# Performance work log

Hardware: AMD Instinct MI355X
Metric: run time of the kernel (lower is better)

## Reference

```python
import jax, jax.numpy as jnp
import numpy as np
from jax import lax

B, T, C = 512, 128, 66
H, L, W = 512, 2, 10


def gru_cell(x, h, W_ih, W_hh, b_ih, b_hh):
    # PyTorch GRU gate order: r, z, n
    gi = x @ W_ih.T + b_ih            # [B, 3H]
    gh = h @ W_hh.T + b_hh            # [B, 3H]
    i_r, i_z, i_n = jnp.split(gi, 3, axis=-1)
    h_r, h_z, h_n = jnp.split(gh, 3, axis=-1)
    r = jax.nn.sigmoid(i_r + h_r)
    z = jax.nn.sigmoid(i_z + h_z)
    n = jnp.tanh(i_n + r * h_n)
    return (1.0 - z) * n + z * h


def setup_inputs() -> dict:
    key = jax.random.key(0)
    ks = jax.random.split(key, 16)
    s = 0.02
    inp = {
        "x": jax.random.normal(ks[0], (B, T, C), jnp.float32),
        # GRU layer 0 (input C -> hidden H)
        "W_ih0": jax.random.normal(ks[1], (3 * H, C), jnp.float32) * s,
        "W_hh0": jax.random.normal(ks[2], (3 * H, H), jnp.float32) * s,
        "b_ih0": jnp.zeros((3 * H,), jnp.float32),
        "b_hh0": jnp.zeros((3 * H,), jnp.float32),
        # GRU layer 1 (hidden H -> hidden H)
        "W_ih1": jax.random.normal(ks[3], (3 * H, H), jnp.float32) * s,
        "W_hh1": jax.random.normal(ks[4], (3 * H, H), jnp.float32) * s,
        "b_ih1": jnp.zeros((3 * H,), jnp.float32),
        "b_hh1": jnp.zeros((3 * H,), jnp.float32),
        # temporal_fc: Linear(window_size, 1) -> weight [1, W], bias [1]
        "temporal_w": jax.random.normal(ks[5], (1, W), jnp.float32) * s,
        "temporal_b": jnp.zeros((1,), jnp.float32),
        # spatial_fc: Linear(H, C)
        "spatial_w": jax.random.normal(ks[6], (C, H), jnp.float32) * s,
        "spatial_b": jnp.zeros((C,), jnp.float32),
    }
    return inp


def _forward(x, W_ih0, W_hh0, b_ih0, b_hh0, W_ih1, W_hh1, b_ih1, b_hh1,
             temporal_w, temporal_b, spatial_w, spatial_b):
    p0 = (W_ih0, W_hh0, b_ih0, b_hh0)
    p1 = (W_ih1, W_hh1, b_ih1, b_hh1)

    # ---- encoder: 2-layer GRU over the full sequence ----
    xs = jnp.transpose(x, (1, 0, 2))  # [T, B, C]
    h0 = jnp.zeros((x.shape[0], H), x.dtype)

    def make_step(p):
        def step(h, xt):
            hn = gru_cell(xt, h, *p)
            return hn, hn
        return step

    hT0, ys0 = lax.scan(make_step(p0), h0, xs)          # ys0 [T,B,H]
    hT1, ys1 = lax.scan(make_step(p1), h0, ys0)         # ys1 [T,B,H]

    encoder_window = jnp.transpose(ys1[-W:], (1, 0, 2))  # [B, W, H]
    last_input_frame = x[:, -1, :]                       # [B, C]

    def dec_step(carry, _):
        (h_0, h_1), win, dec_in = carry
        h_0n = gru_cell(dec_in, h_0, *p0)
        h_1n = gru_cell(h_0n, h_1, *p1)                  # decoder_out [B,H]
        win = jnp.concatenate([win[:, 1:, :], h_1n[:, None, :]], axis=1)
        # temporal_fc over window axis: [B,W,H] -> [B,H]
        t = jnp.einsum('bwh,w->bh', win, temporal_w[0]) + temporal_b[0]
        frame = t @ spatial_w.T + spatial_b + dec_in     # recursive residual
        return ((h_0n, h_1n), win, frame), frame

    init = ((hT0, hT1), encoder_window, last_input_frame)
    _, frames = lax.scan(dec_step, init, None, length=T)  # [T,B,C]
    return jnp.transpose(frames, (1, 0, 2))               # [B,T,C]


def reference(x, W_ih0, W_hh0, b_ih0, b_hh0, W_ih1, W_hh1, b_ih1, b_hh1,
              temporal_w, temporal_b, spatial_w, spatial_b):
    return _forward(x, W_ih0, W_hh0, b_ih0, b_hh0, W_ih1, W_hh1, b_ih1, b_hh1,
                    temporal_w, temporal_b, spatial_w, spatial_b)
```

## Files before the change

### kernel.cpp

```cpp
#include <hip/hip_runtime.h>
#include <hip/hip_bf16.h>

typedef __attribute__((ext_vector_type(8))) short bf16x8;
typedef __attribute__((ext_vector_type(4))) float f32x4;

#define NB 512
#define NT 128
#define NC 66
#define NH 512
#define NW 10
#define CP 96
#define BM 32
#define BJ 64
#define BK 32
#define BKP 40
#define NWG 256
#define NTHR 256
#define G3 1536

struct Params {
  const float *x, *Wih0, *Whh0, *bih0, *bhh0, *Wih1, *Whh1, *bih1, *bhh1, *tw, *tb, *sw, *sb;
  float *out;
  unsigned *barL, *barG;
  __hip_bfloat16 *Wih0h, *Wih0l;
  __hip_bfloat16 *Wch, *Wcl;
  float *cb;
  float *h0, *h1, *tvec;
  __hip_bfloat16 *winb;
};

__device__ __forceinline__ float sigmoidf_(float x) { return 1.f / (1.f + __expf(-x)); }
__device__ __forceinline__ float tanhf_(float x) {
  float e = __expf(2.f * x);
  return (e - 1.f) / (e + 1.f);
}
__device__ __forceinline__ void split2(float v, __hip_bfloat16& h, __hip_bfloat16& l) {
  h = __float2bfloat16(v);
  l = __float2bfloat16(v - __bfloat162float(h));
}
__device__ __forceinline__ unsigned short bfbits(__hip_bfloat16 h) { return *(unsigned short*)&h; }
__device__ __forceinline__ void splitpack4(float4 v, ushort4& ph, ushort4& pl) {
  __hip_bfloat16 h, l;
  split2(v.x, h, l); ph.x = bfbits(h); pl.x = bfbits(l);
  split2(v.y, h, l); ph.y = bfbits(h); pl.y = bfbits(l);
  split2(v.z, h, l); ph.z = bfbits(h); pl.z = bfbits(l);
  split2(v.w, h, l); ph.w = bfbits(h); pl.w = bfbits(l);
}

__device__ __forceinline__ float4 cload4(const float* p) {
  unsigned long long a = __hip_atomic_load((const unsigned long long*)p,       __ATOMIC_RELAXED, __HIP_MEMORY_SCOPE_AGENT);
  unsigned long long b = __hip_atomic_load(((const unsigned long long*)p) + 1, __ATOMIC_RELAXED, __HIP_MEMORY_SCOPE_AGENT);
  float4 r;
  ((unsigned long long*)&r)[0] = a;
  ((unsigned long long*)&r)[1] = b;
  return r;
}

__device__ __forceinline__ void gbar(unsigned* barL, unsigned* barG, unsigned& phase,
                                     int tid, int grp) {
  __syncthreads();
  ++phase;
  if (tid == 0) {
    unsigned old = __hip_atomic_fetch_add(&barL[grp * 32], 1u, __ATOMIC_RELEASE,
                                          __HIP_MEMORY_SCOPE_AGENT);
    if (old == phase * 32 - 1)
      __hip_atomic_fetch_add(barG, 1u, __ATOMIC_RELAXED, __HIP_MEMORY_SCOPE_AGENT);
    while (__hip_atomic_load(barG, __ATOMIC_RELAXED, __HIP_MEMORY_SCOPE_AGENT) < phase)
      __builtin_amdgcn_s_sleep(2);
  }
  __syncthreads();
  asm volatile("" ::: "memory");
}

#define AM_X 0
#define AM_H 2

__device__ __forceinline__ float4 loadA(int amode, const float* __restrict__ A, int tstep,
                                        int b0, int am, int k) {
  if (amode == AM_X) {
    const float* xr = A + ((size_t)(b0 + am) * NT + tstep) * NC;
    float4 v;
    v.x = (k + 0 < NC) ? xr[k + 0] : 0.f;
    v.y = (k + 1 < NC) ? xr[k + 1] : 0.f;
    v.z = (k + 2 < NC) ? xr[k + 2] : 0.f;
    v.w = (k + 3 < NC) ? xr[k + 3] : 0.f;
    return v;
  }
  return cload4(A + (size_t)(b0 + am) * NH + k);
}

__device__ __forceinline__ void zacc(f32x4 acc[2][4]) {
#pragma unroll
  for (int i = 0; i < 2; ++i)
#pragma unroll
    for (int g = 0; g < 4; ++g) {
      acc[i][g][0] = 0.f; acc[i][g][1] = 0.f; acc[i][g][2] = 0.f; acc[i][g][3] = 0.f;
    }
}

template <int G2, bool PSW>
__device__ __forceinline__ void gemm_tile(
    f32x4 acc[2][4],
    const __hip_bfloat16* __restrict__ Wh, const __hip_bfloat16* __restrict__ Wl,
    const float* __restrict__ Wf, int Kb,
    int amode, const float* __restrict__ A, int tstep,
    int b0, int j0,
    __hip_bfloat16* AsH, __hip_bfloat16* AsL,
    __hip_bfloat16* BsH, __hip_bfloat16* BsL,
    int tid)
{
  const int wv = tid >> 6, lane = tid & 63, quad = lane >> 4, l15 = lane & 15;
  const int ms = wv & 1, jh = wv >> 1;
  const int am = tid >> 3;
  const int ak = (tid & 7) << 2;
  const int nk = Kb >> 5;

  uint4 bh_[3], bl_[3];
  float4 w0_[3], w1_[3];

  auto fetchB = [&](int st) {
    const int kb = st << 5;
#pragma unroll
    for (int r = 0; r < 3; ++r) {
      const int l = tid + r * NTHR;
      const int nl = l >> 2, k8 = (l & 3) << 3;
      const int g = nl >> 6, jl = nl & 63;
      if (PSW) {
        const size_t o = (size_t)(g * NH + j0 + jl) * Kb + kb + k8;
        bh_[r] = *(const uint4*)(Wh + o);
        bl_[r] = *(const uint4*)(Wl + o);
      } else {
        const float* wp = Wf + (size_t)(g * NH + j0 + jl) * Kb + kb + k8;
        w0_[r] = *(const float4*)wp;
        w1_[r] = *(const float4*)(wp + 4);
      }
    }
  };

  float4 av = loadA(amode, A, tstep, b0, am, ak);
  fetchB(0);

  for (int st = 0; st < nk; ++st) {
    const int cur = st & 1;
    __hip_bfloat16* ah_d = AsH + cur * (BM * BKP);
    __hip_bfloat16* al_d = AsL + cur * (BM * BKP);
    __hip_bfloat16* bh_d = BsH + cur * (3 * BJ * BKP);
    __hip_bfloat16* bl_d = BsL + cur * (3 * BJ * BKP);
    {
      ushort4 ph, pl;
      splitpack4(av, ph, pl);
      *(ushort4*)(ah_d + am * BKP + ak) = ph;
      *(ushort4*)(al_d + am * BKP + ak) = pl;
    }
#pragma unroll
    for (int r = 0; r < 3; ++r) {
      const int l = tid + r * NTHR;
      const int nl = l >> 2, k8 = (l & 3) << 3;
      if (PSW) {
        *(uint4*)(bh_d + nl * BKP + k8) = bh_[r];
        *(uint4*)(bl_d + nl * BKP + k8) = bl_[r];
      } else {
        ushort4 ph0, pl0, ph1, pl1;
        splitpack4(w0_[r], ph0, pl0);
        splitpack4(w1_[r], ph1, pl1);
        *(ushort4*)(bh_d + nl * BKP + k8) = ph0;
        *(ushort4*)(bh_d + nl * BKP + k8 + 4) = ph1;
        *(ushort4*)(bl_d + nl * BKP + k8) = pl0;
        *(ushort4*)(bl_d + nl * BKP + k8 + 4) = pl1;
      }
    }
    if (st + 1 < nk) {
      av = loadA(amode, A, tstep, b0, am, ((st + 1) << 5) + ak);
      fetchB(st + 1);
    }
    __syncthreads();
    bf16x8 ah = *(const bf16x8*)(ah_d + (ms * 16 + l15) * BKP + quad * 8);
    bf16x8 al = *(const bf16x8*)(al_d + (ms * 16 + l15) * BKP + quad * 8);
#pragma unroll
    for (int jlf = 0; jlf < 2; ++jlf) {
      const int nbase = (jh * 32 + jlf * 16 + l15) * BKP + quad * 8;
      {
        bf16x8 bh = *(const bf16x8*)(bh_d + nbase);
        bf16x8 bl = *(const bf16x8*)(bl_d + nbase);
        acc[jlf][0] = __builtin_amdgcn_mfma_f32_16x16x32_bf16(ah, bh, acc[jlf][0], 0, 0, 0);
        acc[jlf][0] = __builtin_amdgcn_mfma_f32_16x16x32_bf16(al, bh, acc[jlf][0], 0, 0, 0);
        acc[jlf][0] = __builtin_amdgcn_mfma_f32_16x16x32_bf16(ah, bl, acc[jlf][0], 0, 0, 0);
      }
      {
        bf16x8 bh = *(const bf16x8*)(bh_d + BJ * BKP + nbase);
        bf16x8 bl = *(const bf16x8*)(bl_d + BJ * BKP + nbase);
        acc[jlf][1] = __builtin_amdgcn_mfma_f32_16x16x32_bf16(ah, bh, acc[jlf][1], 0, 0, 0);
        acc[jlf][1] = __builtin_amdgcn_mfma_f32_16x16x32_bf16(al, bh, acc[jlf][1], 0, 0, 0);
        acc[jlf][1] = __builtin_amdgcn_mfma_f32_16x16x32_bf16(ah, bl, acc[jlf][1], 0, 0, 0);
      }
      {
        bf16x8 bh = *(const bf16x8*)(bh_d + 2 * BJ * BKP + nbase);
        bf16x8 bl = *(const bf16x8*)(bl_d + 2 * BJ * BKP + nbase);
        acc[jlf][G2] = __builtin_amdgcn_mfma_f32_16x16x32_bf16(ah, bh, acc[jlf][G2], 0, 0, 0);
        acc[jlf][G2] = __builtin_amdgcn_mfma_f32_16x16x32_bf16(al, bh, acc[jlf][G2], 0, 0, 0);
        acc[jlf][G2] = __builtin_amdgcn_mfma_f32_16x16x32_bf16(ah, bl, acc[jlf][G2], 0, 0, 0);
      }
    }
  }
  __syncthreads();
}

__device__ __forceinline__ void ew_gru(
    f32x4 acc[2][4],
    const float* __restrict__ bi, const float* __restrict__ bh,
    const float* __restrict__ hold, float* __restrict__ hnew,
    int b0, int j0, int tid, __hip_bfloat16* win, int slot)
{
  const int wv = tid >> 6, lane = tid & 63, quad = lane >> 4, l15 = lane & 15;
  const int ms = wv & 1, jh = wv >> 1;
#pragma unroll
  for (int jlf = 0; jlf < 2; ++jlf) {
    const int j = j0 + jh * 32 + jlf * 16 + l15;
    const float br = bi[j] + bh[j];
    const float bz = bi[NH + j] + bh[NH + j];
    const float bni = bi[2 * NH + j];
    const float bnh = bh[2 * NH + j];
#pragma unroll
    for (int rg = 0; rg < 4; ++rg) {
      const int b = b0 + ms * 16 + quad * 4 + rg;
      const float r = sigmoidf_(acc[jlf][0][rg] + br);
      const float z = sigmoidf_(acc[jlf][1][rg] + bz);
      const float n = tanhf_(acc[jlf][2][rg] + bni + r * (acc[jlf][3][rg] + bnh));
      const float h = hold[(size_t)b * NH + j];
      const float hn = (1.f - z) * n + z * h;
      hnew[(size_t)b * NH + j] = hn;
      if (win) win[((size_t)b * NW + slot) * NH + j] = __float2bfloat16(hn);
    }
  }
}

__device__ __forceinline__ void ew_dec1(
    f32x4 acc[2][4], const Params& P, float* __restrict__ h1p,
    int b0, int j0, int tid, int s)
{
  const int wv = tid >> 6, lane = tid & 63, quad = lane >> 4, l15 = lane & 15;
  const int ms = wv & 1, jh = wv >> 1;
  const int slot = s % NW;
  float twv[NW];
#pragma unroll
  for (int k = 0; k < NW; ++k) {
    int idx = k - slot - 1; if (idx < 0) idx += NW;
    twv[k] = P.tw[idx];
  }
  const float tw9 = P.tw[NW - 1];
  const float tb0 = P.tb[0];
#pragma unroll
  for (int jlf = 0; jlf < 2; ++jlf) {
    const int j = j0 + jh * 32 + jlf * 16 + l15;
    const float br = P.bih1[j] + P.bhh1[j];
    const float bz = P.bih1[NH + j] + P.bhh1[NH + j];
    const float bni = P.bih1[2 * NH + j];
    const float bnh = P.bhh1[2 * NH + j];
#pragma unroll
    for (int rg = 0; rg < 4; ++rg) {
      const int b = b0 + ms * 16 + quad * 4 + rg;
      const float r = sigmoidf_(acc[jlf][0][rg] + br);
      const float z = sigmoidf_(acc[jlf][1][rg] + bz);
      const float n = tanhf_(acc[jlf][2][rg] + bni + r * (acc[jlf][3][rg] + bnh));
      const float h = h1p[(size_t)b * NH + j];
      const float hn = (1.f - z) * n + z * h;
      h1p[(size_t)b * NH + j] = hn;
      __hip_bfloat16* wrow = P.winb + (size_t)b * NW * NH + j;
      wrow[(size_t)slot * NH] = __float2bfloat16(hn);
      float ts = tb0 + hn * tw9;
#pragma unroll
      for (int k = 0; k < NW; ++k) {
        if (k == slot) continue;
        ts += __bfloat162float(wrow[(size_t)k * NH]) * twv[k];
      }
      P.tvec[(size_t)b * NH + j] = ts;
    }
  }
}

__global__ __launch_bounds__(NTHR) void rnn_kernel(Params P) {
  __shared__ __align__(16) __hip_bfloat16 AsH[2 * BM * BKP];
  __shared__ __align__(16) __hip_bfloat16 AsL[2 * BM * BKP];
  __shared__ __align__(16) __hip_bfloat16 BsH[2 * 3 * BJ * BKP];
  __shared__ __align__(16) __hip_bfloat16 BsL[2 * 3 * BJ * BKP];
  __shared__ __align__(16) float tl[4 * NH];
  const int tid = threadIdx.x;
  const int wg = blockIdx.x;
  const int grp = wg & 7;
  const size_t gid = (size_t)wg * NTHR + tid;
  const size_t GT = (size_t)NWG * NTHR;
  unsigned phase = 0;
  const int wv = tid >> 6, lane = tid & 63, l15 = lane & 15;
  const int jh = wv >> 1;

  for (size_t i = gid; i < (size_t)G3 * CP; i += GT) {
    const int row = (int)(i / CP), k = (int)(i - (size_t)row * CP);
    split2(k < NC ? P.Wih0[(size_t)row * NC + k] : 0.f, P.Wih0h[i], P.Wih0l[i]);
  }
  for (size_t i = gid; i < (size_t)G3 * NH; i += GT) {
    const int r = (int)(i >> 9), h = (int)(i & (NH - 1));
    float a = 0.f;
    for (int c = 0; c < NC; ++c) a += P.Wih0[(size_t)r * NC + c] * P.sw[(size_t)c * NH + h];
    split2(a, P.Wch[i], P.Wcl[i]);
  }
  for (size_t i = gid; i < (size_t)G3; i += GT) {
    float a = 0.f;
    for (int c = 0; c < NC; ++c) a += P.Wih0[i * NC + c] * P.sb[c];
    P.cb[i] = a;
  }
  for (size_t i = gid; i < (size_t)2 * NB * NH; i += GT) { P.h0[i] = 0.f; P.h1[i] = 0.f; }
  gbar(P.barL, P.barG, phase, tid, grp);

  const bool isL1 = wg >= 128;
  const int tile = wg & 127;
  const int b0 = (tile >> 3) * BM;
  const int j0 = (tile & 7) * BJ;

  float G[2][3][4];

  for (int t = 0; t <= NT; ++t) {
    const int cur = t & 1;
    float* h0c = P.h0 + (size_t)cur * NB * NH;
    float* h0n = P.h0 + (size_t)(cur ^ 1) * NB * NH;
    float* h1c = P.h1 + (size_t)cur * NB * NH;
    float* h1n = P.h1 + (size_t)(cur ^ 1) * NB * NH;
    f32x4 acc[2][4];
    if (!isL1) {
      if (t < NT) {
        zacc(acc);
        gemm_tile<2, true>(acc, P.Wih0h, P.Wih0l, nullptr, CP, AM_X, P.x, t, b0, j0, AsH, AsL, BsH, BsL, tid);
        gemm_tile<3, false>(acc, nullptr, nullptr, P.Whh0, NH, AM_H, h0c, 0, b0, j0, AsH, AsL, BsH, BsL, tid);
        ew_gru(acc, P.bih0, P.bhh0, h0c, h0n, b0, j0, tid, nullptr, 0);
      } else {
        zacc(acc);
        gemm_tile<2, true>(acc, P.Wih0h, P.Wih0l, nullptr, CP, AM_X, P.x, NT - 1, b0, j0, AsH, AsL, BsH, BsL, tid);
#pragma unroll
        for (int jlf = 0; jlf < 2; ++jlf)
#pragma unroll
          for (int c = 0; c < 3; ++c)
#pragma unroll
            for (int rg = 0; rg < 4; ++rg) G[jlf][c][rg] = acc[jlf][c][rg];
      }
    } else {
      if (t >= 1) {
        zacc(acc);
        gemm_tile<2, false>(acc, nullptr, nullptr, P.Wih1, NH, AM_H, h0c, 0, b0, j0, AsH, AsL, BsH, BsL, tid);
        gemm_tile<3, false>(acc, nullptr, nullptr, P.Whh1, NH, AM_H, h1c, 0, b0, j0, AsH, AsL, BsH, BsL, tid);
        ew_gru(acc, P.bih1, P.bhh1, h1c, h1n, b0, j0, tid,
               (t >= 119) ? P.winb : nullptr, t - 119);
      }
    }
    gbar(P.barL, P.barG, phase, tid, grp);
  }

  int d0 = 0;
  float* h1p = P.h1 + (size_t)NB * NH;

  float cbr[2][3];
  float Freg[2];
  if (!isL1) {
#pragma unroll
    for (int jlf = 0; jlf < 2; ++jlf)
#pragma unroll
      for (int c = 0; c < 3; ++c)
        cbr[jlf][c] = P.cb[c * NH + j0 + jh * 32 + jlf * 16 + l15];
#pragma unroll
    for (int v = 0; v < 2; ++v) {
      const int t2 = tid + v * NTHR;
      if (t2 < 4 * NC) {
        const int bl = t2 / NC, c = t2 - bl * NC, b = wg * 4 + bl;
        Freg[v] = P.x[((size_t)b * NT + (NT - 1)) * NC + c];
      }
    }
  }

  auto frame_out = [&](int sout) {
    const float* tvb = P.tvec + (size_t)wg * 4 * NH;
    *(float4*)&tl[tid * 8] = cload4(tvb + tid * 8);
    *(float4*)&tl[tid * 8 + 4] = cload4(tvb + tid * 8 + 4);
    __syncthreads();
#pragma unroll
    for (int v = 0; v < 2; ++v) {
      const int t2 = tid + v * NTHR;
      if (t2 < 4 * NC) {
        const int bl = t2 / NC, c = t2 - bl * NC, b = wg * 4 + bl;
        float f = Freg[v] + P.sb[c];
        const float4* swr = (const float4*)(P.sw + (size_t)c * NH);
        const float4* tr = (const float4*)(tl + bl * NH);
#pragma unroll 8
        for (int h4 = 0; h4 < NH / 4; ++h4) {
          float4 tv = tr[h4], wv4 = swr[h4];
          f += tv.x * wv4.x + tv.y * wv4.y + tv.z * wv4.z + tv.w * wv4.w;
        }
        Freg[v] = f;
        P.out[((size_t)b * NT + sout) * NC + c] = f;
      }
    }
    __syncthreads();
  };

  for (int s = 0; s < NT; ++s) {
    float* h0c = P.h0 + (size_t)d0 * NB * NH;
    float* h0n = P.h0 + (size_t)(d0 ^ 1) * NB * NH;
    f32x4 acc[2][4];
    if (!isL1) {
      if (s >= 1) frame_out(s - 1);
      zacc(acc);
      if (s >= 1)
        gemm_tile<2, true>(acc, P.Wch, P.Wcl, nullptr, NH, AM_H, P.tvec, 0, b0, j0, AsH, AsL, BsH, BsL, tid);
#pragma unroll
      for (int jlf = 0; jlf < 2; ++jlf)
#pragma unroll
        for (int c = 0; c < 3; ++c)
#pragma unroll
          for (int rg = 0; rg < 4; ++rg) {
            float g = G[jlf][c][rg] + acc[jlf][c][rg] + (s >= 1 ? cbr[jlf][c] : 0.f);
            G[jlf][c][rg] = g;
            acc[jlf][c][rg] = g;
          }
      gemm_tile<3, false>(acc, nullptr, nullptr, P.Whh0, NH, AM_H, h0c, 0, b0, j0, AsH, AsL, BsH, BsL, tid);
      ew_gru(acc, P.bih0, P.bhh0, h0c, h0n, b0, j0, tid, nullptr, 0);
    } else {
      zacc(acc);
      gemm_tile<3, false>(acc, nullptr, nullptr, P.Whh1, NH, AM_H, h1p, 0, b0, j0, AsH, AsL, BsH, BsL, tid);
    }
    gbar(P.barL, P.barG, phase, tid, grp);
    if (isL1) {
      gemm_tile<2, false>(acc, nullptr, nullptr, P.Wih1, NH, AM_H, h0n, 0, b0, j0, AsH, AsL, BsH, BsL, tid);
      ew_dec1(acc, P, h1p, b0, j0, tid, s);
    }
    gbar(P.barL, P.barG, phase, tid, grp);
    d0 ^= 1;
  }
  if (!isL1) frame_out(NT - 1);
}

extern "C" void kernel_launch(void* const* d_in, const int* in_sizes, int n_in,
                              void* d_out, int out_size, void* d_ws, size_t ws_size,
                              hipStream_t stream) {
  (void)in_sizes; (void)n_in; (void)out_size; (void)ws_size;
  Params P;
  P.x    = (const float*)d_in[0];
  P.Wih0 = (const float*)d_in[1];
  P.Whh0 = (const float*)d_in[2];
  P.bih0 = (const float*)d_in[3];
  P.bhh0 = (const float*)d_in[4];
  P.Wih1 = (const float*)d_in[5];
  P.Whh1 = (const float*)d_in[6];
  P.bih1 = (const float*)d_in[7];
  P.bhh1 = (const float*)d_in[8];
  P.tw   = (const float*)d_in[9];
  P.tb   = (const float*)d_in[10];
  P.sw   = (const float*)d_in[11];
  P.sb   = (const float*)d_in[12];
  P.out  = (float*)d_out;

  char* w = (char*)d_ws;
  size_t used = 0;
  auto take = [&](size_t bytes) {
    char* p = w + used;
    used += (bytes + 255) & ~(size_t)255;
    return p;
  };
  unsigned* bar = (unsigned*)take(2048);
  P.barL = bar;
  P.barG = bar + 8 * 32;
  P.Wih0h = (__hip_bfloat16*)take((size_t)G3 * CP * 2);
  P.Wih0l = (__hip_bfloat16*)take((size_t)G3 * CP * 2);
  P.Wch   = (__hip_bfloat16*)take((size_t)G3 * NH * 2);
  P.Wcl   = (__hip_bfloat16*)take((size_t)G3 * NH * 2);
  P.cb    = (float*)take((size_t)G3 * 4);
  P.h0    = (float*)take((size_t)2 * NB * NH * 4);
  P.h1    = (float*)take((size_t)2 * NB * NH * 4);
  P.tvec  = (float*)take((size_t)NB * NH * 4);
  P.winb  = (__hip_bfloat16*)take((size_t)NB * NW * NH * 2);

  hipMemsetAsync(d_ws, 0, 2048, stream);
  rnn_kernel<<<dim3(NWG), dim3(NTHR), 0, stream>>>(P);
}
```

Baseline: 15.84 ms.

## Pre-split weights into MFMA fragment layout and drop LDS staging in GEMMs

Measured after the change: 14.62 ms. 7.7% less time.

```diff
diff --git a/kernel.cpp b/kernel.cpp
--- a/kernel.cpp
+++ b/kernel.cpp
@@ -12,11 +12,11 @@
 #define CP 96
 #define BM 32
 #define BJ 64
-#define BK 32
-#define BKP 40
 #define NWG 256
 #define NTHR 256
 #define G3 1536
+#define NKS_H 16
+#define NKS_X 3
 
 struct Params {
   const float *x, *Wih0, *Whh0, *bih0, *bhh0, *Wih1, *Whh1, *bih1, *bhh1, *tw, *tb, *sw, *sb;
@@ -24,6 +24,9 @@
   unsigned *barL, *barG;
   __hip_bfloat16 *Wih0h, *Wih0l;
   __hip_bfloat16 *Wch, *Wcl;
+  __hip_bfloat16 *Whh0H, *Whh0L;
+  __hip_bfloat16 *Wih1H, *Wih1L;
+  __hip_bfloat16 *Whh1H, *Whh1L;
   float *cb;
   float *h0, *h1, *tvec;
   __hip_bfloat16 *winb;
@@ -75,20 +78,6 @@
 #define AM_X 0
 #define AM_H 2
 
-__device__ __forceinline__ float4 loadA(int amode, const float* __restrict__ A, int tstep,
-                                        int b0, int am, int k) {
-  if (amode == AM_X) {
-    const float* xr = A + ((size_t)(b0 + am) * NT + tstep) * NC;
-    float4 v;
-    v.x = (k + 0 < NC) ? xr[k + 0] : 0.f;
-    v.y = (k + 1 < NC) ? xr[k + 1] : 0.f;
-    v.z = (k + 2 < NC) ? xr[k + 2] : 0.f;
-    v.w = (k + 3 < NC) ? xr[k + 3] : 0.f;
-    return v;
-  }
-  return cload4(A + (size_t)(b0 + am) * NH + k);
-}
-
 __device__ __forceinline__ void zacc(f32x4 acc[2][4]) {
 #pragma unroll
   for (int i = 0; i < 2; ++i)
@@ -98,111 +87,88 @@
     }
 }
 
-template <int G2, bool PSW>
-__device__ __forceinline__ void gemm_tile(
+template <int G2, int AMODE>
+__device__ __forceinline__ void gemm_frag(
     f32x4 acc[2][4],
-    const __hip_bfloat16* __restrict__ Wh, const __hip_bfloat16* __restrict__ Wl,
-    const float* __restrict__ Wf, int Kb,
-    int amode, const float* __restrict__ A, int tstep,
-    int b0, int j0,
-    __hip_bfloat16* AsH, __hip_bfloat16* AsL,
-    __hip_bfloat16* BsH, __hip_bfloat16* BsL,
-    int tid)
+    const __hip_bfloat16* __restrict__ WH, const __hip_bfloat16* __restrict__ WL,
+    const int nks,
+    const float* __restrict__ A, int tstep, int b0, int j0, int tid)
 {
   const int wv = tid >> 6, lane = tid & 63, quad = lane >> 4, l15 = lane & 15;
   const int ms = wv & 1, jh = wv >> 1;
-  const int am = tid >> 3;
-  const int ak = (tid & 7) << 2;
-  const int nk = Kb >> 5;
-
-  uint4 bh_[3], bl_[3];
-  float4 w0_[3], w1_[3];
-
-  auto fetchB = [&](int st) {
-    const int kb = st << 5;
-#pragma unroll
-    for (int r = 0; r < 3; ++r) {
-      const int l = tid + r * NTHR;
-      const int nl = l >> 2, k8 = (l & 3) << 3;
-      const int g = nl >> 6, jl = nl & 63;
-      if (PSW) {
-        const size_t o = (size_t)(g * NH + j0 + jl) * Kb + kb + k8;
-        bh_[r] = *(const uint4*)(Wh + o);
-        bl_[r] = *(const uint4*)(Wl + o);
-      } else {
-        const float* wp = Wf + (size_t)(g * NH + j0 + jl) * Kb + kb + k8;
-        w0_[r] = *(const float4*)wp;
-        w1_[r] = *(const float4*)(wp + 4);
-      }
+  const int arow = b0 + ms * 16 + l15;
+
+  unsigned boff[6];
+#pragma unroll
+  for (int c = 0; c < 3; ++c)
+#pragma unroll
+    for (int jl = 0; jl < 2; ++jl) {
+      const int jb = c * 32 + (j0 >> 4) + jh * 2 + jl;
+      boff[c * 2 + jl] = (unsigned)((jb * nks) * 64 + lane) * 8u;
+    }
+
+  const float* arp = (AMODE == AM_X)
+      ? A + ((size_t)arow * NT + tstep) * NC
+      : A + (size_t)arow * NH + (quad << 3);
+
+  uint4 bh0[6], bl0[6], bh1[6], bl1[6];
+  float a0[8], a1[8];
+
+  auto loadB = [&](uint4 (&bh)[6], uint4 (&bl)[6], int st) {
+    const unsigned so = (unsigned)st * 512u;
+#pragma unroll
+    for (int f = 0; f < 6; ++f) {
+      bh[f] = *(const uint4*)(WH + boff[f] + so);
+      bl[f] = *(const uint4*)(WL + boff[f] + so);
     }
   };
-
-  float4 av = loadA(amode, A, tstep, b0, am, ak);
-  fetchB(0);
-
-  for (int st = 0; st < nk; ++st) {
-    const int cur = st & 1;
-    __hip_bfloat16* ah_d = AsH + cur * (BM * BKP);
-    __hip_bfloat16* al_d = AsL + cur * (BM * BKP);
-    __hip_bfloat16* bh_d = BsH + cur * (3 * BJ * BKP);
-    __hip_bfloat16* bl_d = BsL + cur * (3 * BJ * BKP);
-    {
-      ushort4 ph, pl;
-      splitpack4(av, ph, pl);
-      *(ushort4*)(ah_d + am * BKP + ak) = ph;
-      *(ushort4*)(al_d + am * BKP + ak) = pl;
-    }
-#pragma unroll
-    for (int r = 0; r < 3; ++r) {
-      const int l = tid + r * NTHR;
-      const int nl = l >> 2, k8 = (l & 3) << 3;
-      if (PSW) {
-        *(uint4*)(bh_d + nl * BKP + k8) = bh_[r];
-        *(uint4*)(bl_d + nl * BKP + k8) = bl_[r];
-      } else {
-        ushort4 ph0, pl0, ph1, pl1;
-        splitpack4(w0_[r], ph0, pl0);
-        splitpack4(w1_[r], ph1, pl1);
-        *(ushort4*)(bh_d + nl * BKP + k8) = ph0;
-        *(ushort4*)(bh_d + nl * BKP + k8 + 4) = ph1;
-        *(ushort4*)(bl_d + nl * BKP + k8) = pl0;
-        *(ushort4*)(bl_d + nl * BKP + k8 + 4) = pl1;
-      }
-    }
-    if (st + 1 < nk) {
-      av = loadA(amode, A, tstep, b0, am, ((st + 1) << 5) + ak);
-      fetchB(st + 1);
-    }
-    __syncthreads();
-    bf16x8 ah = *(const bf16x8*)(ah_d + (ms * 16 + l15) * BKP + quad * 8);
-    bf16x8 al = *(const bf16x8*)(al_d + (ms * 16 + l15) * BKP + quad * 8);
-#pragma unroll
-    for (int jlf = 0; jlf < 2; ++jlf) {
-      const int nbase = (jh * 32 + jlf * 16 + l15) * BKP + quad * 8;
-      {
-        bf16x8 bh = *(const bf16x8*)(bh_d + nbase);
-        bf16x8 bl = *(const bf16x8*)(bl_d + nbase);
-        acc[jlf][0] = __builtin_amdgcn_mfma_f32_16x16x32_bf16(ah, bh, acc[jlf][0], 0, 0, 0);
-        acc[jlf][0] = __builtin_amdgcn_mfma_f32_16x16x32_bf16(al, bh, acc[jlf][0], 0, 0, 0);
-        acc[jlf][0] = __builtin_amdgcn_mfma_f32_16x16x32_bf16(ah, bl, acc[jlf][0], 0, 0, 0);
-      }
-      {
-        bf16x8 bh = *(const bf16x8*)(bh_d + BJ * BKP + nbase);
-        bf16x8 bl = *(const bf16x8*)(bl_d + BJ * BKP + nbase);
-        acc[jlf][1] = __builtin_amdgcn_mfma_f32_16x16x32_bf16(ah, bh, acc[jlf][1], 0, 0, 0);
-        acc[jlf][1] = __builtin_amdgcn_mfma_f32_16x16x32_bf16(al, bh, acc[jlf][1], 0, 0, 0);
-        acc[jlf][1] = __builtin_amdgcn_mfma_f32_16x16x32_bf16(ah, bl, acc[jlf][1], 0, 0, 0);
-      }
-      {
-        bf16x8 bh = *(const bf16x8*)(bh_d + 2 * BJ * BKP + nbase);
-        bf16x8 bl = *(const bf16x8*)(bl_d + 2 * BJ * BKP + nbase);
-        acc[jlf][G2] = __builtin_amdgcn_mfma_f32_16x16x32_bf16(ah, bh, acc[jlf][G2], 0, 0, 0);
-        acc[jlf][G2] = __builtin_amdgcn_mfma_f32_16x16x32_bf16(al, bh, acc[jlf][G2], 0, 0, 0);
-        acc[jlf][G2] = __builtin_amdgcn_mfma_f32_16x16x32_bf16(ah, bl, acc[jlf][G2], 0, 0, 0);
-      }
-    }
-  }
-  __syncthreads();
+  auto loadAfr = [&](float (&a)[8], int st) {
+    if (AMODE == AM_X) {
+      const int k0 = st * 32 + (quad << 3);
+#pragma unroll
+      for (int e = 0; e < 8; ++e) a[e] = (k0 + e < NC) ? arp[k0 + e] : 0.f;
+    } else {
+      const float4 v0 = cload4(arp + st * 32);
+      const float4 v1 = cload4(arp + st * 32 + 4);
+      a[0] = v0.x; a[1] = v0.y; a[2] = v0.z; a[3] = v0.w;
+      a[4] = v1.x; a[5] = v1.y; a[6] = v1.z; a[7] = v1.w;
+    }
+  };
+  auto comp = [&](const uint4 (&bh)[6], const uint4 (&bl)[6], const float (&a)[8]) {
+    float4 v0, v1;
+    v0.x = a[0]; v0.y = a[1]; v0.z = a[2]; v0.w = a[3];
+    v1.x = a[4]; v1.y = a[5]; v1.z = a[6]; v1.w = a[7];
+    ushort4 ph0, pl0, ph1, pl1;
+    splitpack4(v0, ph0, pl0);
+    splitpack4(v1, ph1, pl1);
+    bf16x8 ah, al;
+    ((ushort4*)&ah)[0] = ph0; ((ushort4*)&ah)[1] = ph1;
+    ((ushort4*)&al)[0] = pl0; ((ushort4*)&al)[1] = pl1;
+#pragma unroll
+    for (int jl = 0; jl < 2; ++jl)
+#pragma unroll
+      for (int c = 0; c < 3; ++c) {
+        const int f = c * 2 + jl;
+        const int g = (c == 2) ? G2 : c;
+        const bf16x8 vbh = *(const bf16x8*)&bh[f];
+        const bf16x8 vbl = *(const bf16x8*)&bl[f];
+        acc[jl][g] = __builtin_amdgcn_mfma_f32_16x16x32_bf16(ah, vbh, acc[jl][g], 0, 0, 0);
+        acc[jl][g] = __builtin_amdgcn_mfma_f32_16x16x32_bf16(al, vbh, acc[jl][g], 0, 0, 0);
+        acc[jl][g] = __builtin_amdgcn_mfma_f32_16x16x32_bf16(ah, vbl, acc[jl][g], 0, 0, 0);
+      }
+  };
+
+  loadB(bh0, bl0, 0);
+  loadAfr(a0, 0);
+  if (nks > 1) { loadB(bh1, bl1, 1); loadAfr(a1, 1); }
+  for (int st = 0; st < nks; st += 2) {
+    comp(bh0, bl0, a0);
+    if (st + 2 < nks) { loadB(bh0, bl0, st + 2); loadAfr(a0, st + 2); }
+    if (st + 1 < nks) {
+      comp(bh1, bl1, a1);
+      if (st + 3 < nks) { loadB(bh1, bl1, st + 3); loadAfr(a1, st + 3); }
+    }
+  }
 }
 
 __device__ __forceinline__ void ew_gru(
@@ -279,10 +245,6 @@
 }
 
 __global__ __launch_bounds__(NTHR) void rnn_kernel(Params P) {
-  __shared__ __align__(16) __hip_bfloat16 AsH[2 * BM * BKP];
-  __shared__ __align__(16) __hip_bfloat16 AsL[2 * BM * BKP];
-  __shared__ __align__(16) __hip_bfloat16 BsH[2 * 3 * BJ * BKP];
-  __shared__ __align__(16) __hip_bfloat16 BsL[2 * 3 * BJ * BKP];
   __shared__ __align__(16) float tl[4 * NH];
   const int tid = threadIdx.x;
   const int wg = blockIdx.x;
@@ -293,15 +255,58 @@
   const int wv = tid >> 6, lane = tid & 63, l15 = lane & 15;
   const int jh = wv >> 1;
 
-  for (size_t i = gid; i < (size_t)G3 * CP; i += GT) {
-    const int row = (int)(i / CP), k = (int)(i - (size_t)row * CP);
-    split2(k < NC ? P.Wih0[(size_t)row * NC + k] : 0.f, P.Wih0h[i], P.Wih0l[i]);
-  }
-  for (size_t i = gid; i < (size_t)G3 * NH; i += GT) {
-    const int r = (int)(i >> 9), h = (int)(i & (NH - 1));
-    float a = 0.f;
-    for (int c = 0; c < NC; ++c) a += P.Wih0[(size_t)r * NC + c] * P.sw[(size_t)c * NH + h];
-    split2(a, P.Wch[i], P.Wcl[i]);
+  for (size_t f = gid; f < (size_t)G3 * CP / 8; f += GT) {
+    const int ln = (int)(f & 63), blk = (int)(f >> 6);
+    const int ks = blk % NKS_X, jb = blk / NKS_X;
+    const int r = jb * 16 + (ln & 15);
+    const int k0 = ks * 32 + ((ln >> 4) << 3);
+#pragma unroll
+    for (int e = 0; e < 8; ++e) {
+      const int k = k0 + e;
+      split2(k < NC ? P.Wih0[(size_t)r * NC + k] : 0.f,
+             P.Wih0h[f * 8 + e], P.Wih0l[f * 8 + e]);
+    }
+  }
+  {
+    const float* srcs[3] = { P.Whh0, P.Wih1, P.Whh1 };
+    __hip_bfloat16* dhs[3] = { P.Whh0H, P.Wih1H, P.Whh1H };
+    __hip_bfloat16* dls[3] = { P.Whh0L, P.Wih1L, P.Whh1L };
+#pragma unroll
+    for (int m = 0; m < 3; ++m) {
+      const float* __restrict__ W = srcs[m];
+      __hip_bfloat16* __restrict__ DH = dhs[m];
+      __hip_bfloat16* __restrict__ DL = dls[m];
+      for (size_t f = gid; f < (size_t)G3 * NH / 8; f += GT) {
+        const int ln = (int)(f & 63), blk = (int)(f >> 6);
+        const int ks = blk & 15, jb = blk >> 4;
+        const int r = jb * 16 + (ln & 15);
+        const int k0 = ks * 32 + ((ln >> 4) << 3);
+        const float* src = W + (size_t)r * NH + k0;
+        ushort4 h0v, l0v, h1v, l1v;
+        splitpack4(*(const float4*)(src), h0v, l0v);
+        splitpack4(*(const float4*)(src + 4), h1v, l1v);
+        *(ushort4*)(DH + f * 8)     = h0v;
+        *(ushort4*)(DH + f * 8 + 4) = h1v;
+        *(ushort4*)(DL + f * 8)     = l0v;
+        *(ushort4*)(DL + f * 8 + 4) = l1v;
+      }
+    }
+  }
+  for (size_t f = gid; f < (size_t)G3 * NH / 8; f += GT) {
+    const int ln = (int)(f & 63), blk = (int)(f >> 6);
+    const int ks = blk & 15, jb = blk >> 4;
+    const int r = jb * 16 + (ln & 15);
+    const int k0 = ks * 32 + ((ln >> 4) << 3);
+    float s[8] = {0.f, 0.f, 0.f, 0.f, 0.f, 0.f, 0.f, 0.f};
+    for (int c = 0; c < NC; ++c) {
+      const float a = P.Wih0[(size_t)r * NC + c];
+      const float4 w0 = *(const float4*)(P.sw + (size_t)c * NH + k0);
+      const float4 w1 = *(const float4*)(P.sw + (size_t)c * NH + k0 + 4);
+      s[0] += a * w0.x; s[1] += a * w0.y; s[2] += a * w0.z; s[3] += a * w0.w;
+      s[4] += a * w1.x; s[5] += a * w1.y; s[6] += a * w1.z; s[7] += a * w1.w;
+    }
+#pragma unroll
+    for (int e = 0; e < 8; ++e) split2(s[e], P.Wch[f * 8 + e], P.Wcl[f * 8 + e]);
   }
   for (size_t i = gid; i < (size_t)G3; i += GT) {
     float a = 0.f;
@@ -328,12 +333,12 @@
     if (!isL1) {
       if (t < NT) {
         zacc(acc);
-        gemm_tile<2, true>(acc, P.Wih0h, P.Wih0l, nullptr, CP, AM_X, P.x, t, b0, j0, AsH, AsL, BsH, BsL, tid);
-        gemm_tile<3, false>(acc, nullptr, nullptr, P.Whh0, NH, AM_H, h0c, 0, b0, j0, AsH, AsL, BsH, BsL, tid);
+        gemm_frag<2, AM_X>(acc, P.Wih0h, P.Wih0l, NKS_X, P.x, t, b0, j0, tid);
+        gemm_frag<3, AM_H>(acc, P.Whh0H, P.Whh0L, NKS_H, h0c, 0, b0, j0, tid);
         ew_gru(acc, P.bih0, P.bhh0, h0c, h0n, b0, j0, tid, nullptr, 0);
       } else {
         zacc(acc);
-        gemm_tile<2, true>(acc, P.Wih0h, P.Wih0l, nullptr, CP, AM_X, P.x, NT - 1, b0, j0, AsH, AsL, BsH, BsL, tid);
+        gemm_frag<2, AM_X>(acc, P.Wih0h, P.Wih0l, NKS_X, P.x, NT - 1, b0, j0, tid);
 #pragma unroll
         for (int jlf = 0; jlf < 2; ++jlf)
 #pragma unroll
@@ -344,8 +349,8 @@
     } else {
       if (t >= 1) {
         zacc(acc);
-        gemm_tile<2, false>(acc, nullptr, nullptr, P.Wih1, NH, AM_H, h0c, 0, b0, j0, AsH, AsL, BsH, BsL, tid);
-        gemm_tile<3, false>(acc, nullptr, nullptr, P.Whh1, NH, AM_H, h1c, 0, b0, j0, AsH, AsL, BsH, BsL, tid);
+        gemm_frag<2, AM_H>(acc, P.Wih1H, P.Wih1L, NKS_H, h0c, 0, b0, j0, tid);
+        gemm_frag<3, AM_H>(acc, P.Whh1H, P.Whh1L, NKS_H, h1c, 0, b0, j0, tid);
         ew_gru(acc, P.bih1, P.bhh1, h1c, h1n, b0, j0, tid,
                (t >= 119) ? P.winb : nullptr, t - 119);
       }
@@ -407,7 +412,7 @@
       if (s >= 1) frame_out(s - 1);
       zacc(acc);
       if (s >= 1)
-        gemm_tile<2, true>(acc, P.Wch, P.Wcl, nullptr, NH, AM_H, P.tvec, 0, b0, j0, AsH, AsL, BsH, BsL, tid);
+        gemm_frag<2, AM_H>(acc, P.Wch, P.Wcl, NKS_H, P.tvec, 0, b0, j0, tid);
 #pragma unroll
       for (int jlf = 0; jlf < 2; ++jlf)
 #pragma unroll
@@ -418,15 +423,15 @@
             G[jlf][c][rg] = g;
             acc[jlf][c][rg] = g;
           }
-      gemm_tile<3, false>(acc, nullptr, nullptr, P.Whh0, NH, AM_H, h0c, 0, b0, j0, AsH, AsL, BsH, BsL, tid);
+      gemm_frag<3, AM_H>(acc, P.Whh0H, P.Whh0L, NKS_H, h0c, 0, b0, j0, tid);
       ew_gru(acc, P.bih0, P.bhh0, h0c, h0n, b0, j0, tid, nullptr, 0);
     } else {
       zacc(acc);
-      gemm_tile<3, false>(acc, nullptr, nullptr, P.Whh1, NH, AM_H, h1p, 0, b0, j0, AsH, AsL, BsH, BsL, tid);
+      gemm_frag<3, AM_H>(acc, P.Whh1H, P.Whh1L, NKS_H, h1p, 0, b0, j0, tid);
     }
     gbar(P.barL, P.barG, phase, tid, grp);
     if (isL1) {
-      gemm_tile<2, false>(acc, nullptr, nullptr, P.Wih1, NH, AM_H, h0n, 0, b0, j0, AsH, AsL, BsH, BsL, tid);
+      gemm_frag<2, AM_H>(acc, P.Wih1H, P.Wih1L, NKS_H, h0n, 0, b0, j0, tid);
       ew_dec1(acc, P, h1p, b0, j0, tid, s);
     }
     gbar(P.barL, P.barG, phase, tid, grp);
@@ -469,6 +474,12 @@
   P.Wih0l = (__hip_bfloat16*)take((size_t)G3 * CP * 2);
   P.Wch   = (__hip_bfloat16*)take((size_t)G3 * NH * 2);
   P.Wcl   = (__hip_bfloat16*)take((size_t)G3 * NH * 2);
+  P.Whh0H = (__hip_bfloat16*)take((size_t)G3 * NH * 2);
+  P.Whh0L = (__hip_bfloat16*)take((size_t)G3 * NH * 2);
+  P.Wih1H = (__hip_bfloat16*)take((size_t)G3 * NH * 2);
+  P.Wih1L = (__hip_bfloat16*)take((size_t)G3 * NH * 2);
+  P.Whh1H = (__hip_bfloat16*)take((size_t)G3 * NH * 2);
+  P.Whh1L = (__hip_bfloat16*)take((size_t)G3 * NH * 2);
   P.cb    = (float*)take((size_t)G3 * 4);
   P.h0    = (float*)take((size_t)2 * NB * NH * 4);
   P.h1    = (float*)take((size_t)2 * NB * NH * 4);
```
